# Optimization experiments

Hardware: AMD Instinct MI355X
Metric: run time of the kernel (lower is better)

## Reference

```python
import jax, jax.numpy as jnp
import numpy as np

HIDDEN = 2048
N_HEADS = 16
N_KV = 2
HEAD_DIM = 256
ROT_DIM = 64  # partial_rotary_factor 0.25
EPS = 1e-6
B, S = 2, 2048


def _rms_norm(x, w, eps=EPS):
    var = jnp.mean(jnp.square(x), axis=-1, keepdims=True)
    return x * jax.lax.rsqrt(var + eps) * w


def _rotate_half(x):
    x1, x2 = jnp.split(x, 2, axis=-1)
    return jnp.concatenate([-x2, x1], axis=-1)


def setup_inputs() -> dict:
    key = jax.random.key(0)
    ks = jax.random.split(key, 8)
    hidden_states = jax.random.normal(ks[0], (B, S, HIDDEN), dtype=jnp.float32)
    # real RoPE cos/sin over rotary_dim (HF convention: freqs duplicated)
    inv_freq = 1.0 / (10000.0 ** (np.arange(0, ROT_DIM, 2, dtype=np.float32) / ROT_DIM))
    pos = np.arange(S, dtype=np.float32)
    ang = np.einsum('s,f->sf', pos, inv_freq)                # [S, ROT_DIM/2]
    emb = np.concatenate([ang, ang], axis=-1)                # [S, ROT_DIM]
    cos = jnp.asarray(np.broadcast_to(np.cos(emb), (B, S, ROT_DIM)))
    sin = jnp.asarray(np.broadcast_to(np.sin(emb), (B, S, ROT_DIM)))
    sc = 0.02
    Wq = jax.random.normal(ks[1], (N_HEADS * HEAD_DIM * 2, HIDDEN), dtype=jnp.float32) * sc
    Wk = jax.random.normal(ks[2], (N_KV * HEAD_DIM, HIDDEN), dtype=jnp.float32) * sc
    Wv = jax.random.normal(ks[3], (N_KV * HEAD_DIM, HIDDEN), dtype=jnp.float32) * sc
    Wo = jax.random.normal(ks[4], (HIDDEN, N_HEADS * HEAD_DIM), dtype=jnp.float32) * sc
    q_norm_w = jnp.ones((HEAD_DIM,), dtype=jnp.float32)
    k_norm_w = jnp.ones((HEAD_DIM,), dtype=jnp.float32)
    return {"hidden_states": hidden_states, "cos": cos, "sin": sin,
            "Wq": Wq, "Wk": Wk, "Wv": Wv, "Wo": Wo,
            "q_norm_w": q_norm_w, "k_norm_w": k_norm_w}


def reference(hidden_states, cos, sin, Wq, Wk, Wv, Wo, q_norm_w, k_norm_w):
    b, s, _ = hidden_states.shape
    # gated Q projection: [b, s, n_heads, 2*head_dim] -> query, gate
    qg = jnp.einsum('bsd,od->bso', hidden_states, Wq).reshape(b, s, N_HEADS, 2 * HEAD_DIM)
    q, gate = jnp.split(qg, 2, axis=-1)                      # each [b,s,H,D]
    gate = gate.reshape(b, s, N_HEADS * HEAD_DIM)
    k = jnp.einsum('bsd,od->bso', hidden_states, Wk).reshape(b, s, N_KV, HEAD_DIM)
    v = jnp.einsum('bsd,od->bso', hidden_states, Wv).reshape(b, s, N_KV, HEAD_DIM)
    # per-head RMSNorm before RoPE
    q = _rms_norm(q, q_norm_w)
    k = _rms_norm(k, k_norm_w)
    # partial RoPE on first ROT_DIM dims
    c = cos[:, :, None, :]
    sn = sin[:, :, None, :]
    q_rot, q_pass = q[..., :ROT_DIM], q[..., ROT_DIM:]
    k_rot, k_pass = k[..., :ROT_DIM], k[..., ROT_DIM:]
    q_rot = q_rot * c + _rotate_half(q_rot) * sn
    k_rot = k_rot * c + _rotate_half(k_rot) * sn
    q = jnp.concatenate([q_rot, q_pass], axis=-1)
    k = jnp.concatenate([k_rot, k_pass], axis=-1)
    # GQA: repeat kv heads
    rep = N_HEADS // N_KV
    k = jnp.repeat(k, rep, axis=2)
    v = jnp.repeat(v, rep, axis=2)
    scale = 1.0 / jnp.sqrt(jnp.float32(HEAD_DIM))
    scores = jnp.einsum('bqhd,bkhd->bhqk', q, k) * scale
    causal = jnp.tril(jnp.ones((s, s), dtype=bool))
    scores = jnp.where(causal[None, None], scores, jnp.finfo(scores.dtype).min)
    probs = jax.nn.softmax(scores, axis=-1)
    attn = jnp.einsum('bhqk,bkhd->bqhd', probs, v).reshape(b, s, N_HEADS * HEAD_DIM)
    attn = attn * jax.nn.sigmoid(gate)
    return jnp.einsum('bsi,oi->bso', attn, Wo)
```

## Files before the change

kernel.cpp:

```cpp
#include <hip/hip_runtime.h>
#include <stdint.h>

typedef unsigned short u16;
typedef __bf16 bf16x8 __attribute__((ext_vector_type(8)));
typedef float f32x4 __attribute__((ext_vector_type(4)));
typedef u16 u16x4 __attribute__((ext_vector_type(4)));
typedef u16 u16x8 __attribute__((ext_vector_type(8)));

__device__ __forceinline__ u16 f2b(float f) {
    unsigned u = __builtin_bit_cast(unsigned, f);
    u = u + 0x7FFFu + ((u >> 16) & 1u);
    return (u16)(u >> 16);
}
__device__ __forceinline__ float b2f(u16 b) {
    return __builtin_bit_cast(float, (unsigned)b << 16);
}

__device__ __forceinline__ void glds16(const u16* g, u16* l) {
    __builtin_amdgcn_global_load_lds(
        (const __attribute__((address_space(1))) void*)g,
        (__attribute__((address_space(3))) void*)l,
        16, 0, 0);
}

__global__ __launch_bounds__(256) void cast_bf16(const float* __restrict__ src,
                                                 u16* __restrict__ dst, int n) {
    int i = (blockIdx.x * 256 + threadIdx.x) * 4;
    if (i >= n) return;
    f32x4 v = *(const f32x4*)(src + i);
    u16x4 o;
    o.x = f2b(v.x); o.y = f2b(v.y); o.z = f2b(v.z); o.w = f2b(v.w);
    *(u16x4*)(dst + i) = o;
}

template <int OUT_BF16>
__global__ __launch_bounds__(256) void gemm_bt(const u16* __restrict__ A,
                                               const u16* __restrict__ Bt,
                                               void* __restrict__ Cout,
                                               int M, int N, int K) {
    __shared__ u16 As[128 * 32];
    __shared__ u16 Bs[128 * 32];
    const int tid  = threadIdx.x;
    const int w    = tid >> 6;
    const int lane = tid & 63;
    const int quad = lane >> 4;
    const int ml   = lane & 15;
    const long bm  = (long)blockIdx.y * 128;
    const long bn  = (long)blockIdx.x * 128;
    const int wm   = (w >> 1) * 64;
    const int wn   = (w & 1) * 64;
    const int grow = lane >> 2;
    const int gcol = (lane & 3) * 8;

    const u16* Ag = A  + (bm + w * 16 + grow) * (long)K + gcol;
    const u16* Bg = Bt + (bn + w * 16 + grow) * (long)K + gcol;
    u16* lAs0 = &As[(w * 16) * 32];
    u16* lAs1 = &As[(64 + w * 16) * 32];
    u16* lBs0 = &Bs[(w * 16) * 32];
    u16* lBs1 = &Bs[(64 + w * 16) * 32];

    const f32x4 fz = {0.f, 0.f, 0.f, 0.f};
    f32x4 acc[4][4];
#pragma unroll
    for (int i = 0; i < 4; ++i)
#pragma unroll
        for (int j = 0; j < 4; ++j) acc[i][j] = fz;

    for (int k0 = 0; k0 < K; k0 += 32) {
        __syncthreads();
        glds16(Ag + k0,               lAs0);
        glds16(Ag + 64 * (long)K + k0, lAs1);
        glds16(Bg + k0,               lBs0);
        glds16(Bg + 64 * (long)K + k0, lBs1);
        __builtin_amdgcn_s_waitcnt(0);
        __syncthreads();
        bf16x8 af[4], bfr[4];
#pragma unroll
        for (int mt = 0; mt < 4; ++mt)
            af[mt] = *(const bf16x8*)&As[(wm + mt * 16 + ml) * 32 + quad * 8];
#pragma unroll
        for (int nt = 0; nt < 4; ++nt)
            bfr[nt] = *(const bf16x8*)&Bs[(wn + nt * 16 + ml) * 32 + quad * 8];
#pragma unroll
        for (int mt = 0; mt < 4; ++mt)
#pragma unroll
            for (int nt = 0; nt < 4; ++nt)
                acc[mt][nt] = __builtin_amdgcn_mfma_f32_16x16x32_bf16(
                    af[mt], bfr[nt], acc[mt][nt], 0, 0, 0);
    }
#pragma unroll
    for (int mt = 0; mt < 4; ++mt)
#pragma unroll
        for (int nt = 0; nt < 4; ++nt)
#pragma unroll
            for (int r = 0; r < 4; ++r) {
                long row = bm + wm + mt * 16 + quad * 4 + r;
                long col = bn + wn + nt * 16 + ml;
                float v = acc[mt][nt][r];
                if (OUT_BF16) ((u16*)Cout)[row * N + col] = f2b(v);
                else          ((float*)Cout)[row * N + col] = v;
            }
}

__global__ __launch_bounds__(64) void norm_rope(const u16* __restrict__ qgk,
                                                const float* __restrict__ cosp,
                                                const float* __restrict__ sinp,
                                                const float* __restrict__ qw,
                                                const float* __restrict__ kw,
                                                u16* __restrict__ qf,
                                                u16* __restrict__ kf) {
    const int t = blockIdx.x;
    const int u = blockIdx.y;
    const int lane = threadIdx.x;
    const int b = t >> 11, s = t & 2047;
    const u16* src; const float* wgt; u16* dst;
    if (u < 16) {
        src = qgk + (long)t * 8704 + u * 512;
        wgt = qw;
        dst = qf + ((long)(b * 16 + u) * 2048 + s) * 256;
    } else {
        int kh = u - 16;
        src = qgk + (long)t * 8704 + 8192 + kh * 256;
        wgt = kw;
        dst = kf + ((long)(b * 2 + kh) * 2048 + s) * 256;
    }
    const int d0 = lane * 4;
    u16x4 raw = *(const u16x4*)(src + d0);
    float x0 = b2f(raw.x), x1 = b2f(raw.y), x2 = b2f(raw.z), x3 = b2f(raw.w);
    float ss = x0 * x0 + x1 * x1 + x2 * x2 + x3 * x3;
    for (int off = 32; off; off >>= 1) ss += __shfl_xor(ss, off, 64);
    float inv = rsqrtf(ss * (1.0f / 256.0f) + 1e-6f);
    float n0 = x0 * inv * wgt[d0 + 0];
    float n1 = x1 * inv * wgt[d0 + 1];
    float n2 = x2 * inv * wgt[d0 + 2];
    float n3 = x3 * inv * wgt[d0 + 3];
    float p0 = __shfl_xor(n0, 8, 64);
    float p1 = __shfl_xor(n1, 8, 64);
    float p2 = __shfl_xor(n2, 8, 64);
    float p3 = __shfl_xor(n3, 8, 64);
    if (lane < 16) {
        f32x4 c  = *(const f32x4*)(cosp + (long)t * 64 + d0);
        f32x4 sn = *(const f32x4*)(sinp + (long)t * 64 + d0);
        float sgn = (lane < 8) ? -1.f : 1.f;
        n0 = n0 * c[0] + sgn * p0 * sn[0];
        n1 = n1 * c[1] + sgn * p1 * sn[1];
        n2 = n2 * c[2] + sgn * p2 * sn[2];
        n3 = n3 * c[3] + sgn * p3 * sn[3];
    }
    const float qs = (u < 16) ? 0.0625f : 1.0f;
    n0 *= qs; n1 *= qs; n2 *= qs; n3 *= qs;
    u16x4 o;
    o.x = f2b(n0); o.y = f2b(n1); o.z = f2b(n2); o.w = f2b(n3);
    *(u16x4*)(dst + d0) = o;
}

__global__ __launch_bounds__(256, 2) void attn_fused(const u16* __restrict__ qf,
                                                     const u16* __restrict__ kf,
                                                     const u16* __restrict__ vt,
                                                     const u16* __restrict__ qgk,
                                                     u16* __restrict__ attn_g) {
    __shared__ u16 Ks[64 * 264];
    __shared__ u16 Vt[256 * 72];
    __shared__ u16 P[64 * 72];
    const int flat = blockIdx.x;
    const int qt = 31 - (flat >> 5);
    const int h  = flat & 15;
    const int b  = (flat >> 4) & 1;
    const int kh = h >> 3;
    const int tid = threadIdx.x;
    const int w = tid >> 6, lane = tid & 63;
    const int quad = lane >> 4, ml = lane & 15;
    const int qbase = qt * 64;
    const int qrow = qbase + w * 16;

    const u16* qptr = qf + ((long)(b * 16 + h) * 2048 + qrow + ml) * 256;
    bf16x8 qfrag[8];
#pragma unroll
    for (int dd = 0; dd < 8; ++dd)
        qfrag[dd] = *(const bf16x8*)(qptr + dd * 32 + quad * 8);

    const f32x4 fz = {0.f, 0.f, 0.f, 0.f};
    f32x4 oacc[16];
#pragma unroll
    for (int i = 0; i < 16; ++i) oacc[i] = fz;
    float lsum[4] = {0.f, 0.f, 0.f, 0.f};

    const u16* kbp = kf + (long)(b * 2 + kh) * 2048 * 256;
    const long vbase = (long)kh * 256 * 4096 + (long)b * 2048;

    u16x8 Kreg[8], Vreg[8];
#pragma unroll
    for (int i = 0; i < 8; ++i) {
        int c = i * 256 + tid;
        Kreg[i] = *(const u16x8*)(kbp + (long)(c >> 5) * 256 + (c & 31) * 8);
        Vreg[i] = *(const u16x8*)(vt + vbase + (long)(c >> 3) * 4096 + (c & 7) * 8);
    }

    const int nkt = qt + 1;
    for (int kt = 0; kt < nkt; ++kt) {
        __syncthreads();
#pragma unroll
        for (int i = 0; i < 8; ++i) {
            int c = i * 256 + tid;
            *(u16x8*)&Ks[(c >> 5) * 264 + (c & 31) * 8] = Kreg[i];
            *(u16x8*)&Vt[(c >> 3) * 72 + (c & 7) * 8]   = Vreg[i];
        }
        __syncthreads();
        if (kt + 1 < nkt) {
            const int kb2 = (kt + 1) * 64;
#pragma unroll
            for (int i = 0; i < 8; ++i) {
                int c = i * 256 + tid;
                Kreg[i] = *(const u16x8*)(kbp + (long)(kb2 + (c >> 5)) * 256 + (c & 31) * 8);
                Vreg[i] = *(const u16x8*)(vt + vbase + (long)(c >> 3) * 4096 + kb2 + (c & 7) * 8);
            }
        }

        f32x4 sacc[4];
#pragma unroll
        for (int i = 0; i < 4; ++i) sacc[i] = fz;
#pragma unroll
        for (int dd = 0; dd < 8; ++dd) {
            bf16x8 kf0 = *(const bf16x8*)&Ks[(0 * 16 + ml) * 264 + dd * 32 + quad * 8];
            bf16x8 kf1 = *(const bf16x8*)&Ks[(1 * 16 + ml) * 264 + dd * 32 + quad * 8];
            bf16x8 kf2 = *(const bf16x8*)&Ks[(2 * 16 + ml) * 264 + dd * 32 + quad * 8];
            bf16x8 kf3 = *(const bf16x8*)&Ks[(3 * 16 + ml) * 264 + dd * 32 + quad * 8];
            sacc[0] = __builtin_amdgcn_mfma_f32_16x16x32_bf16(qfrag[dd], kf0, sacc[0], 0, 0, 0);
            sacc[1] = __builtin_amdgcn_mfma_f32_16x16x32_bf16(qfrag[dd], kf1, sacc[1], 0, 0, 0);
            sacc[2] = __builtin_amdgcn_mfma_f32_16x16x32_bf16(qfrag[dd], kf2, sacc[2], 0, 0, 0);
            sacc[3] = __builtin_amdgcn_mfma_f32_16x16x32_bf16(qfrag[dd], kf3, sacc[3], 0, 0, 0);
        }

        const bool diag = (kt == qt);
#pragma unroll
        for (int nt = 0; nt < 4; ++nt)
#pragma unroll
            for (int r = 0; r < 4; ++r) {
                float sv = sacc[nt][r];
                if (diag) {
                    int col = nt * 16 + ml;
                    int row = w * 16 + quad * 4 + r;
                    sv = (col > row) ? -1e30f : sv;
                }
                float pv = __expf(sv - 16.0f);
                lsum[r] += pv;
                P[(w * 16 + quad * 4 + r) * 72 + nt * 16 + ml] = f2b(pv);
            }

#pragma unroll
        for (int ks = 0; ks < 2; ++ks) {
            bf16x8 pfrag = *(const bf16x8*)&P[(w * 16 + ml) * 72 + ks * 32 + quad * 8];
#pragma unroll
            for (int dt = 0; dt < 16; ++dt) {
                bf16x8 vfrag = *(const bf16x8*)&Vt[(dt * 16 + ml) * 72 + ks * 32 + quad * 8];
                oacc[dt] = __builtin_amdgcn_mfma_f32_16x16x32_bf16(pfrag, vfrag, oacc[dt], 0, 0, 0);
            }
        }
    }

#pragma unroll
    for (int off = 1; off < 16; off <<= 1)
#pragma unroll
        for (int r = 0; r < 4; ++r) lsum[r] += __shfl_xor(lsum[r], off, 64);

#pragma unroll
    for (int dt = 0; dt < 16; ++dt)
#pragma unroll
        for (int r = 0; r < 4; ++r) {
            int srow = qrow + quad * 4 + r;
            long tok = (long)b * 2048 + srow;
            int d = dt * 16 + ml;
            float o = oacc[dt][r] / lsum[r];
            float g = b2f(qgk[tok * 8704 + h * 512 + 256 + d]);
            float gv = o / (1.f + __expf(-g));
            attn_g[tok * 4096 + h * 256 + d] = f2b(gv);
        }
}

extern "C" void kernel_launch(void* const* d_in, const int* in_sizes, int n_in,
                              void* d_out, int out_size, void* d_ws, size_t ws_size,
                              hipStream_t stream) {
    (void)in_sizes; (void)n_in; (void)out_size;
    const float* hidden = (const float*)d_in[0];
    const float* cosp   = (const float*)d_in[1];
    const float* sinp   = (const float*)d_in[2];
    const float* Wq     = (const float*)d_in[3];
    const float* Wk     = (const float*)d_in[4];
    const float* Wv     = (const float*)d_in[5];
    const float* Wo     = (const float*)d_in[6];
    const float* qw     = (const float*)d_in[7];
    const float* kw     = (const float*)d_in[8];
    float* out = (float*)d_out;

    char* p = (char*)d_ws;
    u16* h_bf   = (u16*)p; p += (size_t)8388608 * 2;
    u16* Wqk_bf = (u16*)p; p += (size_t)17825792 * 2;
    u16* Wv_bf  = (u16*)p; p += (size_t)1048576 * 2;
    u16* Wo_bf  = (u16*)p; p += (size_t)8388608 * 2;
    u16* qgk    = (u16*)p; p += (size_t)35651584 * 2;
    u16* v_t    = (u16*)p; p += (size_t)2097152 * 2;
    u16* q_f    = (u16*)p; p += (size_t)16777216 * 2;
    u16* k_f    = (u16*)p; p += (size_t)2097152 * 2;
    u16* attn_g = (u16*)p; p += (size_t)16777216 * 2;
    if ((size_t)(p - (char*)d_ws) > ws_size) return;

    cast_bf16<<<8192,  256, 0, stream>>>(hidden, h_bf, 8388608);
    cast_bf16<<<16384, 256, 0, stream>>>(Wq, Wqk_bf, 16777216);
    cast_bf16<<<1024,  256, 0, stream>>>(Wk, Wqk_bf + (size_t)8192 * 2048, 1048576);
    cast_bf16<<<1024,  256, 0, stream>>>(Wv, Wv_bf, 1048576);
    cast_bf16<<<8192,  256, 0, stream>>>(Wo, Wo_bf, 8388608);

    gemm_bt<1><<<dim3(68, 32), 256, 0, stream>>>(h_bf, Wqk_bf, qgk, 4096, 8704, 2048);
    gemm_bt<1><<<dim3(32, 4), 256, 0, stream>>>(Wv_bf, h_bf, v_t, 512, 4096, 2048);

    norm_rope<<<dim3(4096, 18), 64, 0, stream>>>(qgk, cosp, sinp, qw, kw, q_f, k_f);

    attn_fused<<<dim3(1024), 256, 0, stream>>>(q_f, k_f, v_t, qgk, attn_g);

    gemm_bt<0><<<dim3(16, 32), 256, 0, stream>>>(attn_g, Wo_bf, out, 4096, 2048, 4096);
}
```

Measured before the change: 673.4 us.

## Add 256-row multi-stage pipelined GEMM with XCD-aware tile mapping for Q/K and output projections

Adds a new GEMM kernel with 256xBN tiles, 512 threads, a 4-buffer LDS ring filled three stages ahead through direct global-to-LDS loads with partial vmcnt waits, swizzled LDS addressing to avoid bank conflicts, XCD-aware workgroup remapping, and setprio around the MFMA bursts. It replaces the old single-buffered 128x128 GEMM for the large QK projection and the output projection. The aim is to hide global load latency behind MFMA work and raise data reuse per tile. In exchange it uses more LDS and registers, which may limit occupancy.

New measurement: 633.6 us. 1.06x faster.

```diff
diff --git a/kernel.cpp b/kernel.cpp
--- a/kernel.cpp
+++ b/kernel.cpp
@@ -21,6 +21,14 @@
         (const __attribute__((address_space(1))) void*)g,
         (__attribute__((address_space(3))) void*)l,
         16, 0, 0);
+}
+
+template <int N> __device__ __forceinline__ void waitvm() {
+    if constexpr (N == 0)      asm volatile("s_waitcnt vmcnt(0)" ::: "memory");
+    else if constexpr (N == 3) asm volatile("s_waitcnt vmcnt(3)" ::: "memory");
+    else if constexpr (N == 4) asm volatile("s_waitcnt vmcnt(4)" ::: "memory");
+    else if constexpr (N == 6) asm volatile("s_waitcnt vmcnt(6)" ::: "memory");
+    else if constexpr (N == 8) asm volatile("s_waitcnt vmcnt(8)" ::: "memory");
 }
 
 __global__ __launch_bounds__(256) void cast_bf16(const float* __restrict__ src,
@@ -68,9 +76,9 @@
 
     for (int k0 = 0; k0 < K; k0 += 32) {
         __syncthreads();
-        glds16(Ag + k0,               lAs0);
+        glds16(Ag + k0,                lAs0);
         glds16(Ag + 64 * (long)K + k0, lAs1);
-        glds16(Bg + k0,               lBs0);
+        glds16(Bg + k0,                lBs0);
         glds16(Bg + 64 * (long)K + k0, lBs1);
         __builtin_amdgcn_s_waitcnt(0);
         __syncthreads();
@@ -92,6 +100,111 @@
     for (int mt = 0; mt < 4; ++mt)
 #pragma unroll
         for (int nt = 0; nt < 4; ++nt)
+#pragma unroll
+            for (int r = 0; r < 4; ++r) {
+                long row = bm + wm + mt * 16 + quad * 4 + r;
+                long col = bn + wn + nt * 16 + ml;
+                float v = acc[mt][nt][r];
+                if (OUT_BF16) ((u16*)Cout)[row * N + col] = f2b(v);
+                else          ((float*)Cout)[row * N + col] = v;
+            }
+}
+
+template <int OUT_BF16, int BN>
+__global__ __launch_bounds__(512, 2) void gemm256(const u16* __restrict__ A,
+                                                  const u16* __restrict__ Bt,
+                                                  void* __restrict__ Cout,
+                                                  int M, int N, int K, int nbx) {
+    (void)M;
+    constexpr int NFRAG = BN / 64;
+    constexpr int ASZ = 256 * 32;
+    constexpr int BSZ = BN * 32;
+    constexpr int LPT = (BN == 256) ? 4 : 3;
+    __shared__ u16 sm[4][ASZ + BSZ];
+
+    const int tid  = threadIdx.x;
+    const int w    = tid >> 6;
+    const int lane = tid & 63;
+    const int quad = lane >> 4;
+    const int ml   = lane & 15;
+    const int wm   = (w >> 2) * 128;
+    const int wn   = (w & 3) * (BN / 4);
+
+    const int nwg = gridDim.x;
+    const int q8 = nwg >> 3, r8 = nwg & 7;
+    const int xcd = blockIdx.x & 7, loc = blockIdx.x >> 3;
+    const int wg  = (xcd < r8 ? xcd * (q8 + 1) : r8 * (q8 + 1) + (xcd - r8) * q8) + loc;
+    const long bm = (long)(wg / nbx) * 256;
+    const long bn = (long)(wg % nbx) * BN;
+
+    const int  srow = w * 16 + (lane >> 2);
+    const int  scc  = (lane & 3) ^ ((lane >> 3) & 3);
+    const u16* Ag0  = A  + (bm + srow) * (long)K + scc * 8;
+    const u16* Ag1  = Ag0 + 128 * (long)K;
+    const u16* Bg0  = Bt + (bn + srow) * (long)K + scc * 8;
+    const u16* Bg1  = (BN == 256) ? Bg0 + 128 * (long)K : Bg0;
+    const int  ldsw = w * 512;
+
+    const int ccr  = quad ^ ((ml >> 1) & 3);
+    const int aoff = (wm + ml) * 32 + ccr * 8;
+    const int boff = (wn + ml) * 32 + ccr * 8;
+
+    const f32x4 fz = {0.f, 0.f, 0.f, 0.f};
+    f32x4 acc[8][NFRAG];
+#pragma unroll
+    for (int i = 0; i < 8; ++i)
+#pragma unroll
+        for (int j = 0; j < NFRAG; ++j) acc[i][j] = fz;
+
+    const int NT = K >> 5;
+
+#define STAGE(tt)                                                      \
+    {                                                                  \
+        u16* base = &sm[(tt) & 3][0];                                  \
+        const long ko = (long)(tt) * 32;                               \
+        glds16(Ag0 + ko, base + ldsw);                                 \
+        glds16(Ag1 + ko, base + 4096 + ldsw);                          \
+        glds16(Bg0 + ko, base + ASZ + ldsw);                           \
+        if (BN == 256) glds16(Bg1 + ko, base + ASZ + 4096 + ldsw);     \
+    }
+
+    STAGE(0); STAGE(1); STAGE(2);
+
+    for (int t = 0; t < NT; ++t) {
+        if (t < NT - 2)       waitvm<2 * LPT>();
+        else if (t == NT - 2) waitvm<LPT>();
+        else                  waitvm<0>();
+        __builtin_amdgcn_s_barrier();
+        __builtin_amdgcn_sched_barrier(0);
+        if (t + 3 < NT) STAGE(t + 3);
+
+        const u16* Ab = &sm[t & 3][0];
+        const u16* Bb = Ab + ASZ;
+        bf16x8 af[8];
+#pragma unroll
+        for (int mt = 0; mt < 8; ++mt)
+            af[mt] = *(const bf16x8*)(Ab + aoff + mt * 512);
+#pragma unroll
+        for (int nh = 0; nh < NFRAG / 2; ++nh) {
+            bf16x8 b0 = *(const bf16x8*)(Bb + boff + (2 * nh + 0) * 512);
+            bf16x8 b1 = *(const bf16x8*)(Bb + boff + (2 * nh + 1) * 512);
+            __builtin_amdgcn_s_setprio(1);
+#pragma unroll
+            for (int mt = 0; mt < 8; ++mt) {
+                acc[mt][2 * nh]     = __builtin_amdgcn_mfma_f32_16x16x32_bf16(
+                    af[mt], b0, acc[mt][2 * nh], 0, 0, 0);
+                acc[mt][2 * nh + 1] = __builtin_amdgcn_mfma_f32_16x16x32_bf16(
+                    af[mt], b1, acc[mt][2 * nh + 1], 0, 0, 0);
+            }
+            __builtin_amdgcn_s_setprio(0);
+        }
+    }
+#undef STAGE
+
+#pragma unroll
+    for (int mt = 0; mt < 8; ++mt)
+#pragma unroll
+        for (int nt = 0; nt < NFRAG; ++nt)
 #pragma unroll
             for (int r = 0; r < 4; ++r) {
                 long row = bm + wm + mt * 16 + quad * 4 + r;
@@ -310,12 +423,12 @@
     cast_bf16<<<1024,  256, 0, stream>>>(Wv, Wv_bf, 1048576);
     cast_bf16<<<8192,  256, 0, stream>>>(Wo, Wo_bf, 8388608);
 
-    gemm_bt<1><<<dim3(68, 32), 256, 0, stream>>>(h_bf, Wqk_bf, qgk, 4096, 8704, 2048);
+    gemm256<1, 256><<<dim3(544), 512, 0, stream>>>(h_bf, Wqk_bf, qgk, 4096, 8704, 2048, 34);
     gemm_bt<1><<<dim3(32, 4), 256, 0, stream>>>(Wv_bf, h_bf, v_t, 512, 4096, 2048);
 
     norm_rope<<<dim3(4096, 18), 64, 0, stream>>>(qgk, cosp, sinp, qw, kw, q_f, k_f);
 
     attn_fused<<<dim3(1024), 256, 0, stream>>>(q_f, k_f, v_t, qgk, attn_g);
 
-    gemm_bt<0><<<dim3(16, 32), 256, 0, stream>>>(attn_g, Wo_bf, out, 4096, 2048, 4096);
-}
+    gemm256<0, 128><<<dim3(256), 512, 0, stream>>>(attn_g, Wo_bf, out, 4096, 2048, 4096, 16);
+}
```
